# Kernel tuning notes

Hardware: AMD Instinct MI355X
Metric: run time of the kernel (lower is better)

The kernel has to match this reference:

```python
import jax, jax.numpy as jnp
import numpy as np

ALPHA = 0.2  # LeakyReLU negative slope

B, K, F = 64, 100, 128   # batch, window_size (=num_nodes), n_features
E = 2 * K                 # embed_dim*2 = 200 (embed_dim defaults to window_size)


def setup_inputs() -> dict:
    key = jax.random.key(0)
    k1, k2, k3, k4, k5 = jax.random.split(key, 5)
    x = jax.random.normal(k1, (B, K, F), dtype=jnp.float32)
    # lin: Linear(2F -> E); store weight as (2F, E) so projection is x @ W
    W = jax.random.normal(k2, (2 * F, E), dtype=jnp.float32) * (1.0 / np.sqrt(2 * F))
    b = jax.random.normal(k3, (E,), dtype=jnp.float32) * 0.01
    # attention vector a: (E, 1) in torch; use (E,)
    a = jax.random.normal(k4, (E,), dtype=jnp.float32) * (1.414 / np.sqrt(E))
    bias = jax.random.normal(k5, (K, K), dtype=jnp.float32) * 0.01
    return {"x": x, "W": W, "b": b, "a": a, "bias": bias}


def reference(x, W, b, a, bias):
    F_ = x.shape[-1]
    # lin(concat(left, right)) == left @ W[:F] + right @ W[F:] + b;
    # compute the two projections once each instead of materializing the
    # (B, K, K, 2F) pairwise concat tensor.
    left_p = jnp.einsum('bkf,fe->bke', x, W[:F_])    # (B, K, E)
    right_p = jnp.einsum('bkf,fe->bke', x, W[F_:])   # (B, K, E)
    pre = left_p[:, :, None, :] + right_p[:, None, :, :] + b  # (B, K, K, E)
    act = jnp.where(pre > 0, pre, ALPHA * pre)                # LeakyReLU
    e = jnp.einsum('bije,e->bij', act, a) + bias              # (B, K, K)
    attention = jax.nn.softmax(e, axis=2)
    h = jax.nn.sigmoid(jnp.einsum('bij,bjf->bif', attention, x))  # (B, K, F)
    return h
```

## Files before the change

### kernel.cpp

```cpp
#include <hip/hip_runtime.h>

typedef _Float16 half_t;
typedef _Float16 h2 __attribute__((ext_vector_type(2)));
typedef unsigned int uint32;

#define K_ 100
#define F_ 128
#define E_ 200

#if defined(__has_builtin)
#if __has_builtin(__builtin_amdgcn_fdot2)
#define FDOT2(a,b,c) __builtin_amdgcn_fdot2((a),(b),(c),false)
#endif
#endif
#ifndef FDOT2
#define FDOT2(a,b,c) fmaf((float)(a).y,(float)(b).y, fmaf((float)(a).x,(float)(b).x,(c)))
#endif

__device__ __forceinline__ h2 bch2(uint32 u){ return __builtin_bit_cast(h2,u); }
__device__ __forceinline__ uint32 pkh2(float a, float b){
  h2 p; p.x=(half_t)a; p.y=(half_t)b; return __builtin_bit_cast(uint32,p);
}

#define LH_OFF 0
#define RH_OFF 640000
#define AH_OFF 1280000
#define WT_OFF 1280128

__global__ __launch_bounds__(256) void k_wt(
    const float* __restrict__ W, const float* __restrict__ avec,
    uint32* __restrict__ ws)
{
  const int t  = threadIdx.x;
  const int e0 = (int)blockIdx.x * 8;
  __shared__ float wtf[256 * 9];

  for (int u = t; u < 2048; u += 256) {
    int f = u >> 3, ec = u & 7;
    wtf[f * 9 + ec] = W[(size_t)f * E_ + e0 + ec];
  }
  if (blockIdx.x == 0 && t < 100)
    ws[AH_OFF + t] = pkh2(avec[2*t], avec[2*t+1]);
  __syncthreads();

  for (int u = t; u < 1024; u += 256) {
    int col16 = u >> 6, f2 = u & 63;
    int side = col16 >> 3, el = col16 & 7;
    int cu = side * 200 + e0 + el;
    int fbase = side * 128;
    ws[WT_OFF + (size_t)cu * 64 + f2] =
        pkh2(wtf[(fbase + 2*f2) * 9 + el], wtf[(fbase + 2*f2 + 1) * 9 + el]);
  }
}

__global__ __launch_bounds__(256) void k_proj(
    const float* __restrict__ x, const float* __restrict__ bvec,
    uint32* __restrict__ ws)
{
  const int t  = threadIdx.x;
  const int r0 = (int)blockIdx.x * 10;

  __shared__ __align__(16) uint32 xsh[10 * 64];

  for (int u = t; u < 640; u += 256) {
    int row = u >> 6, f2 = u & 63;
    const float* xp = x + (size_t)(r0 + row) * F_ + 2 * f2;
    xsh[row * 64 + f2] = pkh2(xp[0], xp[1]);
  }
  __syncthreads();

  if (t < 200) {
    const uint32* wt0 = ws + WT_OFF + (size_t)(2 * t) * 64;
    const uint32* wt1 = wt0 + 64;
    float acc0[10], acc1[10];
    #pragma unroll
    for (int r = 0; r < 10; ++r) { acc0[r] = 0.f; acc1[r] = 0.f; }
    #pragma unroll
    for (int q = 0; q < 16; ++q) {
      uint4 w0 = *(const uint4*)(wt0 + 4 * q);
      uint4 w1 = *(const uint4*)(wt1 + 4 * q);
      #pragma unroll
      for (int r = 0; r < 10; ++r) {
        uint4 xq = *(const uint4*)(xsh + r * 64 + 4 * q);
        acc0[r] = FDOT2(bch2(xq.x), bch2(w0.x), acc0[r]);
        acc0[r] = FDOT2(bch2(xq.y), bch2(w0.y), acc0[r]);
        acc0[r] = FDOT2(bch2(xq.z), bch2(w0.z), acc0[r]);
        acc0[r] = FDOT2(bch2(xq.w), bch2(w0.w), acc0[r]);
        acc1[r] = FDOT2(bch2(xq.x), bch2(w1.x), acc1[r]);
        acc1[r] = FDOT2(bch2(xq.y), bch2(w1.y), acc1[r]);
        acc1[r] = FDOT2(bch2(xq.z), bch2(w1.z), acc1[r]);
        acc1[r] = FDOT2(bch2(xq.w), bch2(w1.w), acc1[r]);
      }
    }
    const bool isR = (t >= 100);
    const int e2 = isR ? (t - 100) : t;
    if (isR) {
      float b0 = bvec[2 * e2], b1 = bvec[2 * e2 + 1];
      #pragma unroll
      for (int r = 0; r < 10; ++r) { acc0[r] += b0; acc1[r] += b1; }
    }
    uint32* dst = ws + (isR ? RH_OFF : LH_OFF);
    #pragma unroll
    for (int r = 0; r < 10; ++r)
      dst[(size_t)(r0 + r) * 100 + e2] = pkh2(acc0[r], acc1[r]);
  }
}

#define STEP(lu, au, r0u, r1u, r2u, r3u)                                   \
  do {                                                                     \
    h2 a2 = bch2(au); h2 l2 = bch2(lu); h2 rr, mm;                         \
    al = FDOT2(a2, l2, al);                                                \
    rr = bch2(r0u); ar[0] = FDOT2(a2, rr, ar[0]);                          \
    mm = __builtin_elementwise_min(l2 + rr, z2); acc[0] = FDOT2(a2, mm, acc[0]); \
    rr = bch2(r1u); ar[1] = FDOT2(a2, rr, ar[1]);                          \
    mm = __builtin_elementwise_min(l2 + rr, z2); acc[1] = FDOT2(a2, mm, acc[1]); \
    rr = bch2(r2u); ar[2] = FDOT2(a2, rr, ar[2]);                          \
    mm = __builtin_elementwise_min(l2 + rr, z2); acc[2] = FDOT2(a2, mm, acc[2]); \
    rr = bch2(r3u); ar[3] = FDOT2(a2, rr, ar[3]);                          \
    mm = __builtin_elementwise_min(l2 + rr, z2); acc[3] = FDOT2(a2, mm, acc[3]); \
  } while (0)

__global__ __launch_bounds__(640) void k_main(
    const float* __restrict__ x, const float* __restrict__ bias,
    const uint32* __restrict__ ws, float* __restrict__ out)
{
  const int t  = threadIdx.x;
  const int i0 = (int)blockIdx.x * 25;
  const int b  = (int)blockIdx.y;

  __shared__ float  att[2500];
  __shared__ uint32 att2[1250];
  __shared__ float  scratch[640];
  __shared__ float  rowmax[25], rowinv[25];

  const bool act = (t < 625);
  const int ti = act ? (t % 25) : 0;
  const int tj = act ? (t / 25) : 0;

  const uint32* Lrow = ws + LH_OFF + (size_t)(b*K_ + i0 + ti) * 100;
  const uint32* R0   = ws + RH_OFF + (size_t)(b*K_ + tj) * 100;
  const uint32* Ap   = ws + AH_OFF;

  float acc[4] = {0.f,0.f,0.f,0.f};
  float ar[4]  = {0.f,0.f,0.f,0.f};
  float al = 0.f;
  h2 z2; z2.x = (half_t)0; z2.y = (half_t)0;

  #pragma unroll
  for (int g = 0; g < 12; ++g) {
    const int ba = 8*g;
    uint4 La = *(const uint4*)(Lrow + ba),      Lb = *(const uint4*)(Lrow + ba + 4);
    uint4 Aa = *(const uint4*)(Ap + ba),        Ab = *(const uint4*)(Ap + ba + 4);
    uint4 R0a = *(const uint4*)(R0 + ba),       R0b = *(const uint4*)(R0 + ba + 4);
    uint4 R1a = *(const uint4*)(R0 + 2500+ba),  R1b = *(const uint4*)(R0 + 2500+ba+4);
    uint4 R2a = *(const uint4*)(R0 + 5000+ba),  R2b = *(const uint4*)(R0 + 5000+ba+4);
    uint4 R3a = *(const uint4*)(R0 + 7500+ba),  R3b = *(const uint4*)(R0 + 7500+ba+4);
    STEP(La.x, Aa.x, R0a.x, R1a.x, R2a.x, R3a.x);
    STEP(La.y, Aa.y, R0a.y, R1a.y, R2a.y, R3a.y);
    STEP(La.z, Aa.z, R0a.z, R1a.z, R2a.z, R3a.z);
    STEP(La.w, Aa.w, R0a.w, R1a.w, R2a.w, R3a.w);
    STEP(Lb.x, Ab.x, R0b.x, R1b.x, R2b.x, R3b.x);
    STEP(Lb.y, Ab.y, R0b.y, R1b.y, R2b.y, R3b.y);
    STEP(Lb.z, Ab.z, R0b.z, R1b.z, R2b.z, R3b.z);
    STEP(Lb.w, Ab.w, R0b.w, R1b.w, R2b.w, R3b.w);
  }
  {
    uint4 La = *(const uint4*)(Lrow + 96);
    uint4 Aa = *(const uint4*)(Ap + 96);
    uint4 R0a = *(const uint4*)(R0 + 96);
    uint4 R1a = *(const uint4*)(R0 + 2596);
    uint4 R2a = *(const uint4*)(R0 + 5096);
    uint4 R3a = *(const uint4*)(R0 + 7596);
    STEP(La.x, Aa.x, R0a.x, R1a.x, R2a.x, R3a.x);
    STEP(La.y, Aa.y, R0a.y, R1a.y, R2a.y, R3a.y);
    STEP(La.z, Aa.z, R0a.z, R1a.z, R2a.z, R3a.z);
    STEP(La.w, Aa.w, R0a.w, R1a.w, R2a.w, R3a.w);
  }

  float v[4];
  if (act) {
    #pragma unroll
    for (int s = 0; s < 4; ++s) {
      int j = tj + 25*s;
      float lv = al + ar[s] + bias[(i0 + ti)*K_ + j] - 0.8f*acc[s];
      v[s] = fminf(fmaxf(lv, -30000.f), 30000.f);
    }
  }

  {
    float m = -3.0e38f;
    if (act) {
      #pragma unroll
      for (int s = 0; s < 4; ++s) m = fmaxf(m, v[s]);
    }
    scratch[t] = m;
    __syncthreads();
    if (t < 25) {
      float mm = scratch[t];
      for (int k = 1; k < 25; ++k) mm = fmaxf(mm, scratch[t + 25*k]);
      rowmax[t] = mm;
    }
    __syncthreads();
    float ssum = 0.f;
    if (act) {
      float m2 = rowmax[ti];
      #pragma unroll
      for (int s = 0; s < 4; ++s) ssum += __expf(v[s] - m2);
    }
    scratch[t] = ssum;
    __syncthreads();
    if (t < 25) {
      float s2 = 0.f;
      for (int k = 0; k < 25; ++k) s2 += scratch[t + 25*k];
      rowinv[t] = 1.f / s2;
    }
    __syncthreads();
  }
  if (act) {
    float m = rowmax[ti], inv = rowinv[ti];
    #pragma unroll
    for (int s = 0; s < 4; ++s)
      att[ti*K_ + tj + 25*s] = __expf(v[s] - m) * inv;
  }
  __syncthreads();
  for (int u = t; u < 1250; u += 640) {
    int i = u / 50, jp = u - i*50;
    att2[i*50 + jp] = pkh2(att[i*K_ + 2*jp], att[i*K_ + 2*jp + 1]);
  }
  __syncthreads();

  {
    const int f = t & 127, ig = t >> 7;
    float z[5];
    #pragma unroll
    for (int m = 0; m < 5; ++m) z[m] = 0.f;
    const float* xb = x + (size_t)b*K_*F_ + f;
    for (int jp = 0; jp < 50; ++jp) {
      float x0 = xb[(size_t)(2*jp)*F_];
      float x1 = xb[(size_t)(2*jp+1)*F_];
      h2 xv = bch2(pkh2(x0, x1));
      #pragma unroll
      for (int m = 0; m < 5; ++m) {
        h2 av = bch2(att2[(ig + 5*m)*50 + jp]);
        z[m] = FDOT2(av, xv, z[m]);
      }
    }
    #pragma unroll
    for (int m = 0; m < 5; ++m) {
      int i = ig + 5*m;
      out[(size_t)(b*K_ + i0 + i)*F_ + f] = 1.f / (1.f + __expf(-z[m]));
    }
  }
}

extern "C" void kernel_launch(void* const* d_in, const int* in_sizes, int n_in,
                              void* d_out, int out_size, void* d_ws, size_t ws_size,
                              hipStream_t stream)
{
  const float* x    = (const float*)d_in[0];
  const float* W    = (const float*)d_in[1];
  const float* bvec = (const float*)d_in[2];
  const float* avec = (const float*)d_in[3];
  const float* bias = (const float*)d_in[4];
  float* out  = (float*)d_out;
  uint32* ws  = (uint32*)d_ws;

  k_wt  <<<dim3(25),    dim3(256), 0, stream>>>(W, avec, ws);
  k_proj<<<dim3(640),   dim3(256), 0, stream>>>(x, bvec, ws);
  k_main<<<dim3(4, 64), dim3(640), 0, stream>>>(x, bias, ws, out);
}
```

Measured before the change: 102.4 us.

## Retile attention kernel to 5 rows per block for more blocks

Measured after the change: 148.6 us. 45.2% more time.

```diff
diff --git a/kernel.cpp b/kernel.cpp
--- a/kernel.cpp
+++ b/kernel.cpp
@@ -106,7 +106,7 @@
   }
 }
 
-#define STEP(lu, au, r0u, r1u, r2u, r3u)                                   \
+#define STEP2(lu, au, r0u, r1u)                                            \
   do {                                                                     \
     h2 a2 = bch2(au); h2 l2 = bch2(lu); h2 rr, mm;                         \
     al = FDOT2(a2, l2, al);                                                \
@@ -114,74 +114,66 @@
     mm = __builtin_elementwise_min(l2 + rr, z2); acc[0] = FDOT2(a2, mm, acc[0]); \
     rr = bch2(r1u); ar[1] = FDOT2(a2, rr, ar[1]);                          \
     mm = __builtin_elementwise_min(l2 + rr, z2); acc[1] = FDOT2(a2, mm, acc[1]); \
-    rr = bch2(r2u); ar[2] = FDOT2(a2, rr, ar[2]);                          \
-    mm = __builtin_elementwise_min(l2 + rr, z2); acc[2] = FDOT2(a2, mm, acc[2]); \
-    rr = bch2(r3u); ar[3] = FDOT2(a2, rr, ar[3]);                          \
-    mm = __builtin_elementwise_min(l2 + rr, z2); acc[3] = FDOT2(a2, mm, acc[3]); \
   } while (0)
 
-__global__ __launch_bounds__(640) void k_main(
+__global__ __launch_bounds__(256) void k_main(
     const float* __restrict__ x, const float* __restrict__ bias,
     const uint32* __restrict__ ws, float* __restrict__ out)
 {
   const int t  = threadIdx.x;
-  const int i0 = (int)blockIdx.x * 25;
+  const int i0 = (int)blockIdx.x * 5;
   const int b  = (int)blockIdx.y;
 
-  __shared__ float  att[2500];
-  __shared__ uint32 att2[1250];
-  __shared__ float  scratch[640];
-  __shared__ float  rowmax[25], rowinv[25];
-
-  const bool act = (t < 625);
-  const int ti = act ? (t % 25) : 0;
-  const int tj = act ? (t / 25) : 0;
+  __shared__ float  att[500];
+  __shared__ uint32 att2[250];
+  __shared__ float  scratch[256];
+  __shared__ float  rowmax[5], rowinv[5];
+
+  const bool act = (t < 250);
+  const int ti = act ? (t % 5) : 0;
+  const int tj = act ? (t / 5) : 0;
 
   const uint32* Lrow = ws + LH_OFF + (size_t)(b*K_ + i0 + ti) * 100;
   const uint32* R0   = ws + RH_OFF + (size_t)(b*K_ + tj) * 100;
   const uint32* Ap   = ws + AH_OFF;
 
-  float acc[4] = {0.f,0.f,0.f,0.f};
-  float ar[4]  = {0.f,0.f,0.f,0.f};
+  float acc[2] = {0.f, 0.f};
+  float ar[2]  = {0.f, 0.f};
   float al = 0.f;
   h2 z2; z2.x = (half_t)0; z2.y = (half_t)0;
 
   #pragma unroll
   for (int g = 0; g < 12; ++g) {
     const int ba = 8*g;
-    uint4 La = *(const uint4*)(Lrow + ba),      Lb = *(const uint4*)(Lrow + ba + 4);
-    uint4 Aa = *(const uint4*)(Ap + ba),        Ab = *(const uint4*)(Ap + ba + 4);
-    uint4 R0a = *(const uint4*)(R0 + ba),       R0b = *(const uint4*)(R0 + ba + 4);
-    uint4 R1a = *(const uint4*)(R0 + 2500+ba),  R1b = *(const uint4*)(R0 + 2500+ba+4);
-    uint4 R2a = *(const uint4*)(R0 + 5000+ba),  R2b = *(const uint4*)(R0 + 5000+ba+4);
-    uint4 R3a = *(const uint4*)(R0 + 7500+ba),  R3b = *(const uint4*)(R0 + 7500+ba+4);
-    STEP(La.x, Aa.x, R0a.x, R1a.x, R2a.x, R3a.x);
-    STEP(La.y, Aa.y, R0a.y, R1a.y, R2a.y, R3a.y);
-    STEP(La.z, Aa.z, R0a.z, R1a.z, R2a.z, R3a.z);
-    STEP(La.w, Aa.w, R0a.w, R1a.w, R2a.w, R3a.w);
-    STEP(Lb.x, Ab.x, R0b.x, R1b.x, R2b.x, R3b.x);
-    STEP(Lb.y, Ab.y, R0b.y, R1b.y, R2b.y, R3b.y);
-    STEP(Lb.z, Ab.z, R0b.z, R1b.z, R2b.z, R3b.z);
-    STEP(Lb.w, Ab.w, R0b.w, R1b.w, R2b.w, R3b.w);
+    uint4 La = *(const uint4*)(Lrow + ba),     Lb = *(const uint4*)(Lrow + ba + 4);
+    uint4 Aa = *(const uint4*)(Ap + ba),       Ab = *(const uint4*)(Ap + ba + 4);
+    uint4 Ra = *(const uint4*)(R0 + ba),       Rb = *(const uint4*)(R0 + ba + 4);
+    uint4 Sa = *(const uint4*)(R0 + 5000+ba),  Sb = *(const uint4*)(R0 + 5000+ba+4);
+    STEP2(La.x, Aa.x, Ra.x, Sa.x);
+    STEP2(La.y, Aa.y, Ra.y, Sa.y);
+    STEP2(La.z, Aa.z, Ra.z, Sa.z);
+    STEP2(La.w, Aa.w, Ra.w, Sa.w);
+    STEP2(Lb.x, Ab.x, Rb.x, Sb.x);
+    STEP2(Lb.y, Ab.y, Rb.y, Sb.y);
+    STEP2(Lb.z, Ab.z, Rb.z, Sb.z);
+    STEP2(Lb.w, Ab.w, Rb.w, Sb.w);
   }
   {
     uint4 La = *(const uint4*)(Lrow + 96);
     uint4 Aa = *(const uint4*)(Ap + 96);
-    uint4 R0a = *(const uint4*)(R0 + 96);
-    uint4 R1a = *(const uint4*)(R0 + 2596);
-    uint4 R2a = *(const uint4*)(R0 + 5096);
-    uint4 R3a = *(const uint4*)(R0 + 7596);
-    STEP(La.x, Aa.x, R0a.x, R1a.x, R2a.x, R3a.x);
-    STEP(La.y, Aa.y, R0a.y, R1a.y, R2a.y, R3a.y);
-    STEP(La.z, Aa.z, R0a.z, R1a.z, R2a.z, R3a.z);
-    STEP(La.w, Aa.w, R0a.w, R1a.w, R2a.w, R3a.w);
-  }
-
-  float v[4];
+    uint4 Ra = *(const uint4*)(R0 + 96);
+    uint4 Sa = *(const uint4*)(R0 + 5096);
+    STEP2(La.x, Aa.x, Ra.x, Sa.x);
+    STEP2(La.y, Aa.y, Ra.y, Sa.y);
+    STEP2(La.z, Aa.z, Ra.z, Sa.z);
+    STEP2(La.w, Aa.w, Ra.w, Sa.w);
+  }
+
+  float v[2];
   if (act) {
     #pragma unroll
-    for (int s = 0; s < 4; ++s) {
-      int j = tj + 25*s;
+    for (int s = 0; s < 2; ++s) {
+      int j = tj + 50*s;
       float lv = al + ar[s] + bias[(i0 + ti)*K_ + j] - 0.8f*acc[s];
       v[s] = fminf(fmaxf(lv, -30000.f), 30000.f);
     }
@@ -189,66 +181,60 @@
 
   {
     float m = -3.0e38f;
-    if (act) {
-      #pragma unroll
-      for (int s = 0; s < 4; ++s) m = fmaxf(m, v[s]);
-    }
+    if (act) m = fmaxf(v[0], v[1]);
     scratch[t] = m;
     __syncthreads();
-    if (t < 25) {
+    if (t < 5) {
       float mm = scratch[t];
-      for (int k = 1; k < 25; ++k) mm = fmaxf(mm, scratch[t + 25*k]);
+      for (int k = 1; k < 50; ++k) mm = fmaxf(mm, scratch[t + 5*k]);
       rowmax[t] = mm;
     }
     __syncthreads();
     float ssum = 0.f;
     if (act) {
       float m2 = rowmax[ti];
-      #pragma unroll
-      for (int s = 0; s < 4; ++s) ssum += __expf(v[s] - m2);
+      ssum = __expf(v[0] - m2) + __expf(v[1] - m2);
     }
     scratch[t] = ssum;
     __syncthreads();
-    if (t < 25) {
+    if (t < 5) {
       float s2 = 0.f;
-      for (int k = 0; k < 25; ++k) s2 += scratch[t + 25*k];
+      for (int k = 0; k < 50; ++k) s2 += scratch[t + 5*k];
       rowinv[t] = 1.f / s2;
     }
     __syncthreads();
   }
   if (act) {
     float m = rowmax[ti], inv = rowinv[ti];
-    #pragma unroll
-    for (int s = 0; s < 4; ++s)
-      att[ti*K_ + tj + 25*s] = __expf(v[s] - m) * inv;
-  }
-  __syncthreads();
-  for (int u = t; u < 1250; u += 640) {
-    int i = u / 50, jp = u - i*50;
+    att[ti*K_ + tj]      = __expf(v[0] - m) * inv;
+    att[ti*K_ + tj + 50] = __expf(v[1] - m) * inv;
+  }
+  __syncthreads();
+  if (t < 250) {
+    int i = t / 50, jp = t - i*50;
     att2[i*50 + jp] = pkh2(att[i*K_ + 2*jp], att[i*K_ + 2*jp + 1]);
   }
   __syncthreads();
 
   {
     const int f = t & 127, ig = t >> 7;
-    float z[5];
-    #pragma unroll
-    for (int m = 0; m < 5; ++m) z[m] = 0.f;
+    float z[3] = {0.f, 0.f, 0.f};
     const float* xb = x + (size_t)b*K_*F_ + f;
     for (int jp = 0; jp < 50; ++jp) {
       float x0 = xb[(size_t)(2*jp)*F_];
       float x1 = xb[(size_t)(2*jp+1)*F_];
       h2 xv = bch2(pkh2(x0, x1));
       #pragma unroll
-      for (int m = 0; m < 5; ++m) {
-        h2 av = bch2(att2[(ig + 5*m)*50 + jp]);
-        z[m] = FDOT2(av, xv, z[m]);
+      for (int m = 0; m < 3; ++m) {
+        int i = ig + 2*m;
+        if (i < 5) z[m] = FDOT2(bch2(att2[i*50 + jp]), xv, z[m]);
       }
     }
     #pragma unroll
-    for (int m = 0; m < 5; ++m) {
-      int i = ig + 5*m;
-      out[(size_t)(b*K_ + i0 + i)*F_ + f] = 1.f / (1.f + __expf(-z[m]));
+    for (int m = 0; m < 3; ++m) {
+      int i = ig + 2*m;
+      if (i < 5)
+        out[(size_t)(b*K_ + i0 + i)*F_ + f] = 1.f / (1.f + __expf(-z[m]));
     }
   }
 }
@@ -265,7 +251,7 @@
   float* out  = (float*)d_out;
   uint32* ws  = (uint32*)d_ws;
 
-  k_wt  <<<dim3(25),    dim3(256), 0, stream>>>(W, avec, ws);
-  k_proj<<<dim3(640),   dim3(256), 0, stream>>>(x, bvec, ws);
-  k_main<<<dim3(4, 64), dim3(640), 0, stream>>>(x, bias, ws, out);
-}
+  k_wt  <<<dim3(25),     dim3(256), 0, stream>>>(W, avec, ws);
+  k_proj<<<dim3(640),    dim3(256), 0, stream>>>(x, bvec, ws);
+  k_main<<<dim3(20, 64), dim3(256), 0, stream>>>(x, bias, ws, out);
+}
```
